# Optimization experiments

Measured on AMD Instinct MI355X. Metric: run time of the kernel, lower is better.

Reference implementation:

```python
import jax, jax.numpy as jnp
import numpy as np

B = 1024          # batch
L = 200           # max_len (history length)
DIM = 64          # args.dim
ITEM_NUM = 100000 # vocab; table has ITEM_NUM+1 rows, row 0 = padding
NEG = -1e15       # mask additive constant used by the original module


def setup_inputs() -> dict:
    key = jax.random.key(0)
    k1, k2, k3, k4, k5 = jax.random.split(key, 5)
    log_seqs = jax.random.randint(k1, (B, L), 0, ITEM_NUM + 1)          # item ids, 0 = pad
    pred = jax.random.randint(k2, (B, 1), 0, ITEM_NUM + 1)              # gather targets
    item_emb = jax.random.normal(k3, (ITEM_NUM + 1, DIM), jnp.float32) * 0.02
    item_emb = item_emb.at[0].set(0.0)                                  # padding_idx=0
    attn_key = jax.random.uniform(k4, (1, DIM), jnp.float32)            # self.key (torch.rand init)
    pos_emb = jax.random.normal(k5, (L, DIM), jnp.float32) * 0.02       # positional table
    return {"log_seqs": log_seqs, "pred": pred, "item_emb": item_emb,
            "attn_key": attn_key, "pos_emb": pos_emb}


def reference(log_seqs, pred, item_emb, attn_key, pos_emb):
    dim = item_emb.shape[1]
    mask = log_seqs != 0                                  # [B, L] True where valid
    # log2feats (model='P2MAMO', dropout p=0 -> identity)
    seqs = item_emb[log_seqs] * jnp.sqrt(jnp.float32(dim))  # [B, L, D]
    seqs = seqs + pos_emb[None, :, :]
    seqs = seqs * mask[..., None]                         # zero out padded positions
    # single-query dot-product attention pooling with learned key
    sim = jnp.einsum('bld,d->bl', seqs, attn_key[0])      # (q*k).sum(-1)
    sim = sim + jnp.where(mask, 0.0, NEG)                 # sim + (~mask)*-1e15
    attn = jax.nn.softmax(sim, axis=-1)                   # [B, L]
    Q = jnp.einsum('bld,bl->bd', seqs, attn)              # [B, D]
    # training path (isEval=False): full-vocab logits -> softmax -> gather
    logits = Q @ item_emb.T                               # [B, V+1]
    probs = jax.nn.softmax(logits, axis=-1)
    pos_logits = jnp.take_along_axis(probs, pred, axis=1) # [B, 1]
    return pos_logits
```

## Files before the change

kernel.cpp:

```cpp
#include <hip/hip_runtime.h>
#include <math.h>

#define B_TOT   1024
#define L_SEQ   200
#define DIM     64
#define VOCAB   100001
#define NEG_BIG (-1e15f)
#define SEQ_ST16 66
#define LOG2E   1.4426950408889634f
#define EB_SLACK_ROWS 512

typedef __bf16 bf16x8 __attribute__((ext_vector_type(8)));
typedef float  f32x4  __attribute__((ext_vector_type(4)));

static __device__ __forceinline__ float fast_exp2(float x) {
    return __builtin_amdgcn_exp2f(x);
}

__global__ __launch_bounds__(256) void pool_kernel(
    const int*   __restrict__ log_seqs,
    const float* __restrict__ item_emb,
    const float* __restrict__ attn_key,
    const float* __restrict__ pos_emb,
    float*       __restrict__ Q,
    __bf16*      __restrict__ Qb,
    __bf16*      __restrict__ Eb)
{
    const int b    = blockIdx.x;
    const int t    = threadIdx.x;
    const int wave = t >> 6;
    const int lane = t & 63;

    __shared__ unsigned short s_seq16[L_SEQ][SEQ_ST16];
    __shared__ float s_attn[L_SEQ];
    __shared__ float s_red[4];
    __shared__ float s_q[4][DIM];

    float sim = -INFINITY;
    if (t < L_SEQ) {
        const int id = log_seqs[(long)b * L_SEQ + t];
        if (id == 0) {
            sim = NEG_BIG;
            const ushort2 z = make_ushort2(0, 0);
            #pragma unroll
            for (int i = 0; i < DIM / 2; ++i)
                *(ushort2*)&s_seq16[t][2 * i] = z;
        } else {
            float acc = 0.f;
            const float4* e4 = (const float4*)(item_emb + (long)id * DIM);
            const float4* p4 = (const float4*)(pos_emb + t * DIM);
            #pragma unroll
            for (int i = 0; i < DIM / 4; ++i) {
                const float4 e = e4[i];
                const float4 p = p4[i];
                float4 f;
                f.x = fmaf(8.f, e.x, p.x);
                f.y = fmaf(8.f, e.y, p.y);
                f.z = fmaf(8.f, e.z, p.z);
                f.w = fmaf(8.f, e.w, p.w);
                const __bf16 h0 = (__bf16)f.x, h1 = (__bf16)f.y;
                const __bf16 h2 = (__bf16)f.z, h3 = (__bf16)f.w;
                ushort2 u0, u1;
                u0.x = __builtin_bit_cast(unsigned short, h0);
                u0.y = __builtin_bit_cast(unsigned short, h1);
                u1.x = __builtin_bit_cast(unsigned short, h2);
                u1.y = __builtin_bit_cast(unsigned short, h3);
                *(ushort2*)&s_seq16[t][4 * i]     = u0;
                *(ushort2*)&s_seq16[t][4 * i + 2] = u1;
                acc += f.x * attn_key[4*i+0] + f.y * attn_key[4*i+1]
                     + f.z * attn_key[4*i+2] + f.w * attn_key[4*i+3];
            }
            sim = acc;
        }
    }

    float m = sim;
    #pragma unroll
    for (int off = 32; off > 0; off >>= 1) m = fmaxf(m, __shfl_xor(m, off));
    if (lane == 0) s_red[wave] = m;
    __syncthreads();
    m = fmaxf(fmaxf(s_red[0], s_red[1]), fmaxf(s_red[2], s_red[3]));
    __syncthreads();

    float p = (t < L_SEQ) ? __expf(sim - m) : 0.f;
    if (t < L_SEQ) s_attn[t] = p;
    float ls = p;
    #pragma unroll
    for (int off = 32; off > 0; off >>= 1) ls += __shfl_xor(ls, off);
    if (lane == 0) s_red[wave] = ls;
    __syncthreads();
    const float inv = 1.0f / (s_red[0] + s_red[1] + s_red[2] + s_red[3]);

    float q = 0.f;
    const int l0 = wave * (L_SEQ / 4);
    #pragma unroll 2
    for (int l = l0; l < l0 + (L_SEQ / 4); ++l) {
        const unsigned int ui = (unsigned int)s_seq16[l][lane] << 16;
        q = fmaf(s_attn[l], __builtin_bit_cast(float, ui), q);
    }
    s_q[wave][lane] = q;
    __syncthreads();

    if (t < DIM) {
        const float qq = (s_q[0][t] + s_q[1][t] + s_q[2][t] + s_q[3][t]) * inv;
        Q[b * DIM + t]  = qq;
        Qb[b * DIM + t] = (__bf16)(qq * LOG2E);
    }

    {
        const long n8 = ((long)VOCAB * DIM) / 8;
        for (long g = (long)b * 256 + t; g < n8; g += (long)gridDim.x * 256) {
            const long i = g * 8;
            const float4 f0 = ((const float4*)(item_emb + i))[0];
            const float4 f1 = ((const float4*)(item_emb + i))[1];
            bf16x8 o;
            o[0] = (__bf16)f0.x; o[1] = (__bf16)f0.y; o[2] = (__bf16)f0.z; o[3] = (__bf16)f0.w;
            o[4] = (__bf16)f1.x; o[5] = (__bf16)f1.y; o[6] = (__bf16)f1.z; o[7] = (__bf16)f1.w;
            *(bf16x8*)(Eb + i) = o;
        }
    }
}

#define NC        128
#define NBG       8
#define VT_TOTAL  6251
#define VT_FULL   6250
#define VT_PER    49
#define VT_STEP   (16 * 16 * DIM)

__global__ __launch_bounds__(256) void logits_mfma(
    const __bf16* __restrict__ Eb,
    const __bf16* __restrict__ Qb,
    float*        __restrict__ partials)
{
    const int bid   = blockIdx.x;
    const int xcd   = bid & 7;
    const int idx   = bid >> 3;
    const int chunk = xcd + 8 * (idx >> 3);
    const int bg    = idx & 7;
    const int wave  = threadIdx.x >> 6;
    const int lane  = threadIdx.x & 63;
    const int r16   = lane & 15;
    const int hi    = lane >> 4;

    __shared__ float s_part[4][128];

    bf16x8 a[8][2];
    #pragma unroll
    for (int t = 0; t < 8; ++t)
        #pragma unroll
        for (int s = 0; s < 2; ++s)
            a[t][s] = *(const bf16x8*)(Qb + ((bg*128 + t*16 + r16) * DIM) + s*32 + hi*8);

    const int vt0    = chunk * VT_PER;
    const int vt_end = min(vt0 + VT_PER, VT_TOTAL);
    int vt = vt0 + wave;

    float ssum[8][4];
    #pragma unroll
    for (int t = 0; t < 8; ++t)
        #pragma unroll
        for (int r = 0; r < 4; ++r) ssum[t][r] = 0.f;

    #define DO_TILE(c0, c1, v) do {                                           \
        if ((v) < VT_FULL) {                                                  \
            _Pragma("unroll")                                                 \
            for (int t = 0; t < 8; ++t) {                                     \
                f32x4 acc = {0.f, 0.f, 0.f, 0.f};                             \
                acc = __builtin_amdgcn_mfma_f32_16x16x32_bf16(a[t][0], c0, acc, 0, 0, 0); \
                acc = __builtin_amdgcn_mfma_f32_16x16x32_bf16(a[t][1], c1, acc, 0, 0, 0); \
                _Pragma("unroll")                                             \
                for (int r = 0; r < 4; ++r) ssum[t][r] += fast_exp2(acc[r]);  \
            }                                                                 \
        } else {                                                              \
            const bool valid = ((v) * 16 + r16) < VOCAB;                      \
            _Pragma("unroll")                                                 \
            for (int t = 0; t < 8; ++t) {                                     \
                f32x4 acc = {0.f, 0.f, 0.f, 0.f};                             \
                acc = __builtin_amdgcn_mfma_f32_16x16x32_bf16(a[t][0], c0, acc, 0, 0, 0); \
                acc = __builtin_amdgcn_mfma_f32_16x16x32_bf16(a[t][1], c1, acc, 0, 0, 0); \
                _Pragma("unroll")                                             \
                for (int r = 0; r < 4; ++r) ssum[t][r] += valid ? fast_exp2(acc[r]) : 0.f; \
            }                                                                 \
        }                                                                     \
    } while (0)

    const __bf16* base = Eb + ((size_t)vt * 16 + r16) * DIM + hi * 8;
    const __bf16* pA = base;
    const __bf16* pB = base + 4  * 16 * DIM;
    const __bf16* pC = base + 8  * 16 * DIM;
    const __bf16* pD = base + 12 * 16 * DIM;

    bf16x8 A0 = *(const bf16x8*)pA, A1 = *(const bf16x8*)(pA + 32);
    bf16x8 B0 = *(const bf16x8*)pB, B1 = *(const bf16x8*)(pB + 32);
    bf16x8 C0 = *(const bf16x8*)pC, C1 = *(const bf16x8*)(pC + 32);
    bf16x8 D0 = *(const bf16x8*)pD, D1 = *(const bf16x8*)(pD + 32);

    for (;;) {
        DO_TILE(A0, A1, vt);
        if (vt + 4 < vt_end) DO_TILE(B0, B1, vt + 4);
        pA += VT_STEP; pB += VT_STEP;
        A0 = *(const bf16x8*)pA; A1 = *(const bf16x8*)(pA + 32);
        B0 = *(const bf16x8*)pB; B1 = *(const bf16x8*)(pB + 32);
        vt += 8;
        if (vt >= vt_end) break;

        DO_TILE(C0, C1, vt);
        if (vt + 4 < vt_end) DO_TILE(D0, D1, vt + 4);
        pC += VT_STEP; pD += VT_STEP;
        C0 = *(const bf16x8*)pC; C1 = *(const bf16x8*)(pC + 32);
        D0 = *(const bf16x8*)pD; D1 = *(const bf16x8*)(pD + 32);
        vt += 8;
        if (vt >= vt_end) break;
    }
    #undef DO_TILE

    #pragma unroll
    for (int t = 0; t < 8; ++t)
        #pragma unroll
        for (int r = 0; r < 4; ++r) {
            float v = ssum[t][r];
            v += __shfl_xor(v, 1);
            v += __shfl_xor(v, 2);
            v += __shfl_xor(v, 4);
            v += __shfl_xor(v, 8);
            ssum[t][r] = v;
        }

    if (r16 == 0) {
        #pragma unroll
        for (int t = 0; t < 8; ++t)
            #pragma unroll
            for (int r = 0; r < 4; ++r)
                s_part[wave][t * 16 + hi * 4 + r] = ssum[t][r];
    }
    __syncthreads();

    if (threadIdx.x < 128) {
        const int i = threadIdx.x;
        const float v = s_part[0][i] + s_part[1][i] + s_part[2][i] + s_part[3][i];
        partials[(size_t)chunk * B_TOT + bg * 128 + i] = v;
    }
}

__global__ __launch_bounds__(256) void finalize_kernel(
    const float* __restrict__ Q,
    const float* __restrict__ item_emb,
    const int*   __restrict__ pred,
    const float* __restrict__ partials,
    float*       __restrict__ out)
{
    const int b = blockIdx.x * 256 + threadIdx.x;

    float S = 0.f;
    for (int c = 0; c < NC; ++c)
        S += partials[(size_t)c * B_TOT + b];

    const int pv = pred[b];
    float acc = 0.f;
    const float4* e4 = (const float4*)(item_emb + (long)pv * DIM);
    const float4* q4 = (const float4*)(Q + b * DIM);
    #pragma unroll
    for (int i = 0; i < DIM / 4; ++i) {
        const float4 e = e4[i];
        const float4 q = q4[i];
        acc += e.x*q.x + e.y*q.y + e.z*q.z + e.w*q.w;
    }
    out[b] = __expf(acc) / S;
}

extern "C" void kernel_launch(void* const* d_in, const int* in_sizes, int n_in,
                              void* d_out, int out_size, void* d_ws, size_t ws_size,
                              hipStream_t stream)
{
    const int*   log_seqs = (const int*)  d_in[0];
    const int*   pred     = (const int*)  d_in[1];
    const float* item_emb = (const float*)d_in[2];
    const float* attn_key = (const float*)d_in[3];
    const float* pos_emb  = (const float*)d_in[4];
    float*       out      = (float*)d_out;

    char* ws = (char*)d_ws;
    const size_t eb_bytes = (size_t)(VOCAB + EB_SLACK_ROWS) * DIM * 2;
    __bf16* Eb       = (__bf16*)ws;
    __bf16* Qb       = (__bf16*)(ws + eb_bytes);
    float*  Qf       = (float*) (ws + eb_bytes + (size_t)B_TOT * DIM * 2);
    float*  partials = (float*) ((char*)Qf + (size_t)B_TOT * DIM * 4);

    pool_kernel<<<B_TOT, 256, 0, stream>>>(log_seqs, item_emb, attn_key, pos_emb, Qf, Qb, Eb);
    logits_mfma<<<NBG * NC, 256, 0, stream>>>(Eb, Qb, partials);
    finalize_kernel<<<B_TOT / 256, 256, 0, stream>>>(Qf, item_emb, pred, partials, out);
}
```

Before: 64.06 us.

## Fuse fp32-to-bf16 table conversion into the logits MFMA loop

```diff
diff --git a/kernel.cpp b/kernel.cpp
--- a/kernel.cpp
+++ b/kernel.cpp
@@ -8,13 +8,19 @@
 #define NEG_BIG (-1e15f)
 #define SEQ_ST16 66
 #define LOG2E   1.4426950408889634f
-#define EB_SLACK_ROWS 512
 
 typedef __bf16 bf16x8 __attribute__((ext_vector_type(8)));
 typedef float  f32x4  __attribute__((ext_vector_type(4)));
 
 static __device__ __forceinline__ float fast_exp2(float x) {
     return __builtin_amdgcn_exp2f(x);
+}
+
+static __device__ __forceinline__ bf16x8 cvt_bf16x8(const float4 a, const float4 b) {
+    bf16x8 o;
+    o[0] = (__bf16)a.x; o[1] = (__bf16)a.y; o[2] = (__bf16)a.z; o[3] = (__bf16)a.w;
+    o[4] = (__bf16)b.x; o[5] = (__bf16)b.y; o[6] = (__bf16)b.z; o[7] = (__bf16)b.w;
+    return o;
 }
 
 __global__ __launch_bounds__(256) void pool_kernel(
@@ -23,8 +29,7 @@
     const float* __restrict__ attn_key,
     const float* __restrict__ pos_emb,
     float*       __restrict__ Q,
-    __bf16*      __restrict__ Qb,
-    __bf16*      __restrict__ Eb)
+    __bf16*      __restrict__ Qb)
 {
     const int b    = blockIdx.x;
     const int t    = threadIdx.x;
@@ -106,19 +111,6 @@
         Q[b * DIM + t]  = qq;
         Qb[b * DIM + t] = (__bf16)(qq * LOG2E);
     }
-
-    {
-        const long n8 = ((long)VOCAB * DIM) / 8;
-        for (long g = (long)b * 256 + t; g < n8; g += (long)gridDim.x * 256) {
-            const long i = g * 8;
-            const float4 f0 = ((const float4*)(item_emb + i))[0];
-            const float4 f1 = ((const float4*)(item_emb + i))[1];
-            bf16x8 o;
-            o[0] = (__bf16)f0.x; o[1] = (__bf16)f0.y; o[2] = (__bf16)f0.z; o[3] = (__bf16)f0.w;
-            o[4] = (__bf16)f1.x; o[5] = (__bf16)f1.y; o[6] = (__bf16)f1.z; o[7] = (__bf16)f1.w;
-            *(bf16x8*)(Eb + i) = o;
-        }
-    }
 }
 
 #define NC        128
@@ -126,10 +118,9 @@
 #define VT_TOTAL  6251
 #define VT_FULL   6250
 #define VT_PER    49
-#define VT_STEP   (16 * 16 * DIM)
-
-__global__ __launch_bounds__(256) void logits_mfma(
-    const __bf16* __restrict__ Eb,
+
+__global__ __launch_bounds__(256, 3) void logits_mfma(
+    const float*  __restrict__ E,
     const __bf16* __restrict__ Qb,
     float*        __restrict__ partials)
 {
@@ -161,6 +152,15 @@
     for (int t = 0; t < 8; ++t)
         #pragma unroll
         for (int r = 0; r < 4; ++r) ssum[t][r] = 0.f;
+
+    #define LOADB(dst, vti) do {                                              \
+        const int _row = min((vti) * 16 + r16, VOCAB - 1);                    \
+        const float* _p = E + (size_t)_row * DIM + hi * 8;                    \
+        dst[0] = ((const float4*)_p)[0];                                      \
+        dst[1] = ((const float4*)_p)[1];                                      \
+        dst[2] = ((const float4*)(_p + 32))[0];                               \
+        dst[3] = ((const float4*)(_p + 32))[1];                               \
+    } while (0)
 
     #define DO_TILE(c0, c1, v) do {                                           \
         if ((v) < VT_FULL) {                                                  \
@@ -185,35 +185,32 @@
         }                                                                     \
     } while (0)
 
-    const __bf16* base = Eb + ((size_t)vt * 16 + r16) * DIM + hi * 8;
-    const __bf16* pA = base;
-    const __bf16* pB = base + 4  * 16 * DIM;
-    const __bf16* pC = base + 8  * 16 * DIM;
-    const __bf16* pD = base + 12 * 16 * DIM;
-
-    bf16x8 A0 = *(const bf16x8*)pA, A1 = *(const bf16x8*)(pA + 32);
-    bf16x8 B0 = *(const bf16x8*)pB, B1 = *(const bf16x8*)(pB + 32);
-    bf16x8 C0 = *(const bf16x8*)pC, C1 = *(const bf16x8*)(pC + 32);
-    bf16x8 D0 = *(const bf16x8*)pD, D1 = *(const bf16x8*)(pD + 32);
-
-    for (;;) {
-        DO_TILE(A0, A1, vt);
-        if (vt + 4 < vt_end) DO_TILE(B0, B1, vt + 4);
-        pA += VT_STEP; pB += VT_STEP;
-        A0 = *(const bf16x8*)pA; A1 = *(const bf16x8*)(pA + 32);
-        B0 = *(const bf16x8*)pB; B1 = *(const bf16x8*)(pB + 32);
+    float4 bA[4], bB[4];
+    LOADB(bA, vt);
+    LOADB(bB, vt + 4);
+
+    while (vt < vt_end) {
+        float4 cA[4], cB[4];
+        #pragma unroll
+        for (int i = 0; i < 4; ++i) { cA[i] = bA[i]; cB[i] = bB[i]; }
+        const int v0 = vt, v1 = vt + 4;
         vt += 8;
-        if (vt >= vt_end) break;
-
-        DO_TILE(C0, C1, vt);
-        if (vt + 4 < vt_end) DO_TILE(D0, D1, vt + 4);
-        pC += VT_STEP; pD += VT_STEP;
-        C0 = *(const bf16x8*)pC; C1 = *(const bf16x8*)(pC + 32);
-        D0 = *(const bf16x8*)pD; D1 = *(const bf16x8*)(pD + 32);
-        vt += 8;
-        if (vt >= vt_end) break;
+        LOADB(bA, vt);
+        LOADB(bB, vt + 4);
+
+        {
+            const bf16x8 c0 = cvt_bf16x8(cA[0], cA[1]);
+            const bf16x8 c1 = cvt_bf16x8(cA[2], cA[3]);
+            DO_TILE(c0, c1, v0);
+        }
+        if (v1 < vt_end) {
+            const bf16x8 c0 = cvt_bf16x8(cB[0], cB[1]);
+            const bf16x8 c1 = cvt_bf16x8(cB[2], cB[3]);
+            DO_TILE(c0, c1, v1);
+        }
     }
     #undef DO_TILE
+    #undef LOADB
 
     #pragma unroll
     for (int t = 0; t < 8; ++t)
@@ -281,13 +278,11 @@
     float*       out      = (float*)d_out;
 
     char* ws = (char*)d_ws;
-    const size_t eb_bytes = (size_t)(VOCAB + EB_SLACK_ROWS) * DIM * 2;
-    __bf16* Eb       = (__bf16*)ws;
-    __bf16* Qb       = (__bf16*)(ws + eb_bytes);
-    float*  Qf       = (float*) (ws + eb_bytes + (size_t)B_TOT * DIM * 2);
+    __bf16* Qb       = (__bf16*)ws;
+    float*  Qf       = (float*) (ws + (size_t)B_TOT * DIM * 2);
     float*  partials = (float*) ((char*)Qf + (size_t)B_TOT * DIM * 4);
 
-    pool_kernel<<<B_TOT, 256, 0, stream>>>(log_seqs, item_emb, attn_key, pos_emb, Qf, Qb, Eb);
-    logits_mfma<<<NBG * NC, 256, 0, stream>>>(Eb, Qb, partials);
+    pool_kernel<<<B_TOT, 256, 0, stream>>>(log_seqs, item_emb, attn_key, pos_emb, Qf, Qb);
+    logits_mfma<<<NBG * NC, 256, 0, stream>>>(item_emb, Qb, partials);
     finalize_kernel<<<B_TOT / 256, 256, 0, stream>>>(Qf, item_emb, pred, partials, out);
 }
```

Result: slower. 115.9 us (+80.9%).

## Stage item-embedding tiles through LDS with async global_load_lds ring buffer

Applied to the files above, without the earlier changes.

```diff
diff --git a/kernel.cpp b/kernel.cpp
--- a/kernel.cpp
+++ b/kernel.cpp
@@ -12,6 +12,9 @@
 
 typedef __bf16 bf16x8 __attribute__((ext_vector_type(8)));
 typedef float  f32x4  __attribute__((ext_vector_type(4)));
+
+#define GLB_AS __attribute__((address_space(1)))
+#define LDS_AS __attribute__((address_space(3)))
 
 static __device__ __forceinline__ float fast_exp2(float x) {
     return __builtin_amdgcn_exp2f(x);
@@ -126,7 +129,8 @@
 #define VT_TOTAL  6251
 #define VT_FULL   6250
 #define VT_PER    49
-#define VT_STEP   (16 * 16 * DIM)
+#define SLOTS     5
+#define SLOT_B    2048
 
 __global__ __launch_bounds__(256) void logits_mfma(
     const __bf16* __restrict__ Eb,
@@ -143,7 +147,10 @@
     const int r16   = lane & 15;
     const int hi    = lane >> 4;
 
+    __shared__ char  s_stage[4 * SLOTS * SLOT_B];
     __shared__ float s_part[4][128];
+
+    char* wbase = s_stage + wave * (SLOTS * SLOT_B);
 
     bf16x8 a[8][2];
     #pragma unroll
@@ -161,6 +168,18 @@
     for (int t = 0; t < 8; ++t)
         #pragma unroll
         for (int r = 0; r < 4; ++r) ssum[t][r] = 0.f;
+
+    const __bf16* src = Eb + ((size_t)vt * 16 + r16) * DIM + hi * 8;
+
+    #define STAGE(slot, sp) do {                                              \
+        char* _d = wbase + (slot) * SLOT_B;                                   \
+        __builtin_amdgcn_global_load_lds(                                     \
+            (const GLB_AS void*)(const void*)(sp),                            \
+            (LDS_AS void*)(void*)_d, 16, 0, 0);                               \
+        __builtin_amdgcn_global_load_lds(                                     \
+            (const GLB_AS void*)(const void*)((sp) + 32),                     \
+            (LDS_AS void*)(void*)(_d + 1024), 16, 0, 0);                      \
+    } while (0)
 
     #define DO_TILE(c0, c1, v) do {                                           \
         if ((v) < VT_FULL) {                                                  \
@@ -185,35 +204,26 @@
         }                                                                     \
     } while (0)
 
-    const __bf16* base = Eb + ((size_t)vt * 16 + r16) * DIM + hi * 8;
-    const __bf16* pA = base;
-    const __bf16* pB = base + 4  * 16 * DIM;
-    const __bf16* pC = base + 8  * 16 * DIM;
-    const __bf16* pD = base + 12 * 16 * DIM;
-
-    bf16x8 A0 = *(const bf16x8*)pA, A1 = *(const bf16x8*)(pA + 32);
-    bf16x8 B0 = *(const bf16x8*)pB, B1 = *(const bf16x8*)(pB + 32);
-    bf16x8 C0 = *(const bf16x8*)pC, C1 = *(const bf16x8*)(pC + 32);
-    bf16x8 D0 = *(const bf16x8*)pD, D1 = *(const bf16x8*)(pD + 32);
-
-    for (;;) {
-        DO_TILE(A0, A1, vt);
-        if (vt + 4 < vt_end) DO_TILE(B0, B1, vt + 4);
-        pA += VT_STEP; pB += VT_STEP;
-        A0 = *(const bf16x8*)pA; A1 = *(const bf16x8*)(pA + 32);
-        B0 = *(const bf16x8*)pB; B1 = *(const bf16x8*)(pB + 32);
-        vt += 8;
-        if (vt >= vt_end) break;
-
-        DO_TILE(C0, C1, vt);
-        if (vt + 4 < vt_end) DO_TILE(D0, D1, vt + 4);
-        pC += VT_STEP; pD += VT_STEP;
-        C0 = *(const bf16x8*)pC; C1 = *(const bf16x8*)(pC + 32);
-        D0 = *(const bf16x8*)pD; D1 = *(const bf16x8*)(pD + 32);
-        vt += 8;
-        if (vt >= vt_end) break;
+    STAGE(0, src);
+    STAGE(1, src + 4096);
+    STAGE(2, src + 8192);
+    STAGE(3, src + 12288);
+
+    int slot_r = 0, slot_w = 4;
+    while (vt < vt_end) {
+        STAGE(slot_w, src + 16384);
+        if (++slot_w == SLOTS) slot_w = 0;
+        src += 4096;
+        asm volatile("s_waitcnt vmcnt(8)" ::: "memory");
+        const char* rb = wbase + slot_r * SLOT_B + (size_t)lane * 16;
+        const bf16x8 c0 = *(const bf16x8*)rb;
+        const bf16x8 c1 = *(const bf16x8*)(rb + 1024);
+        if (++slot_r == SLOTS) slot_r = 0;
+        DO_TILE(c0, c1, vt);
+        vt += 4;
     }
     #undef DO_TILE
+    #undef STAGE
 
     #pragma unroll
     for (int t = 0; t < 8; ++t)
```

New measurement: 70.29 us. 9.7% more time.

## Split logits blocks into single-wave blocks and drop shared-memory reduction

Applied to the files above, without the earlier changes.

```diff
diff --git a/kernel.cpp b/kernel.cpp
--- a/kernel.cpp
+++ b/kernel.cpp
@@ -126,25 +126,22 @@
 #define VT_TOTAL  6251
 #define VT_FULL   6250
 #define VT_PER    49
-#define VT_STEP   (16 * 16 * DIM)
-
-__global__ __launch_bounds__(256) void logits_mfma(
+
+__global__ __launch_bounds__(64) void logits_mfma(
     const __bf16* __restrict__ Eb,
     const __bf16* __restrict__ Qb,
     float*        __restrict__ partials)
 {
     const int bid   = blockIdx.x;
     const int xcd   = bid & 7;
-    const int idx   = bid >> 3;
-    const int chunk = xcd + 8 * (idx >> 3);
-    const int bg    = idx & 7;
-    const int wave  = threadIdx.x >> 6;
-    const int lane  = threadIdx.x & 63;
+    const int sub   = bid >> 3;
+    const int wslot = sub & 3;
+    const int bg    = (sub >> 2) & 7;
+    const int chunk = xcd + 8 * (sub >> 5);
+    const int lane  = threadIdx.x;
     const int r16   = lane & 15;
     const int hi    = lane >> 4;
 
-    __shared__ float s_part[4][128];
-
     bf16x8 a[8][2];
     #pragma unroll
     for (int t = 0; t < 8; ++t)
@@ -154,7 +151,7 @@
 
     const int vt0    = chunk * VT_PER;
     const int vt_end = min(vt0 + VT_PER, VT_TOTAL);
-    int vt = vt0 + wave;
+    int vt = vt0 + wslot;
 
     float ssum[8][4];
     #pragma unroll
@@ -185,33 +182,26 @@
         }                                                                     \
     } while (0)
 
-    const __bf16* base = Eb + ((size_t)vt * 16 + r16) * DIM + hi * 8;
-    const __bf16* pA = base;
-    const __bf16* pB = base + 4  * 16 * DIM;
-    const __bf16* pC = base + 8  * 16 * DIM;
-    const __bf16* pD = base + 12 * 16 * DIM;
-
-    bf16x8 A0 = *(const bf16x8*)pA, A1 = *(const bf16x8*)(pA + 32);
-    bf16x8 B0 = *(const bf16x8*)pB, B1 = *(const bf16x8*)(pB + 32);
-    bf16x8 C0 = *(const bf16x8*)pC, C1 = *(const bf16x8*)(pC + 32);
-    bf16x8 D0 = *(const bf16x8*)pD, D1 = *(const bf16x8*)(pD + 32);
-
-    for (;;) {
-        DO_TILE(A0, A1, vt);
-        if (vt + 4 < vt_end) DO_TILE(B0, B1, vt + 4);
-        pA += VT_STEP; pB += VT_STEP;
-        A0 = *(const bf16x8*)pA; A1 = *(const bf16x8*)(pA + 32);
-        B0 = *(const bf16x8*)pB; B1 = *(const bf16x8*)(pB + 32);
+    const __bf16* p = Eb + ((size_t)vt * 16 + r16) * DIM + hi * 8;
+
+    bf16x8 b0, b1, d0, d1;
+    b0 = *(const bf16x8*)p;
+    b1 = *(const bf16x8*)(p + 32);
+    d0 = *(const bf16x8*)(p + 4096);
+    d1 = *(const bf16x8*)(p + 4096 + 32);
+
+    while (vt < vt_end) {
+        const bf16x8 c00 = b0, c01 = b1, c10 = d0, c11 = d1;
+        const int v0 = vt, v1 = vt + 4;
         vt += 8;
-        if (vt >= vt_end) break;
-
-        DO_TILE(C0, C1, vt);
-        if (vt + 4 < vt_end) DO_TILE(D0, D1, vt + 4);
-        pC += VT_STEP; pD += VT_STEP;
-        C0 = *(const bf16x8*)pC; C1 = *(const bf16x8*)(pC + 32);
-        D0 = *(const bf16x8*)pD; D1 = *(const bf16x8*)(pD + 32);
-        vt += 8;
-        if (vt >= vt_end) break;
+        p += 8192;
+        b0 = *(const bf16x8*)p;
+        b1 = *(const bf16x8*)(p + 32);
+        d0 = *(const bf16x8*)(p + 4096);
+        d1 = *(const bf16x8*)(p + 4096 + 32);
+
+        DO_TILE(c00, c01, v0);
+        if (v1 < vt_end) DO_TILE(c10, c11, v1);
     }
     #undef DO_TILE
 
@@ -228,18 +218,14 @@
         }
 
     if (r16 == 0) {
+        const int slot = chunk * 4 + wslot;
         #pragma unroll
         for (int t = 0; t < 8; ++t)
             #pragma unroll
-            for (int r = 0; r < 4; ++r)
-                s_part[wave][t * 16 + hi * 4 + r] = ssum[t][r];
-    }
-    __syncthreads();
-
-    if (threadIdx.x < 128) {
-        const int i = threadIdx.x;
-        const float v = s_part[0][i] + s_part[1][i] + s_part[2][i] + s_part[3][i];
-        partials[(size_t)chunk * B_TOT + bg * 128 + i] = v;
+            for (int r = 0; r < 4; ++r) {
+                const int row = bg * 128 + t * 16 + hi * 4 + r;
+                partials[(size_t)slot * B_TOT + row] = ssum[t][r];
+            }
     }
 }
 
@@ -253,8 +239,8 @@
     const int b = blockIdx.x * 256 + threadIdx.x;
 
     float S = 0.f;
-    for (int c = 0; c < NC; ++c)
-        S += partials[(size_t)c * B_TOT + b];
+    for (int w = 0; w < NC * 4; ++w)
+        S += partials[(size_t)w * B_TOT + b];
 
     const int pv = pred[b];
     float acc = 0.f;
@@ -288,6 +274,6 @@
     float*  partials = (float*) ((char*)Qf + (size_t)B_TOT * DIM * 4);
 
     pool_kernel<<<B_TOT, 256, 0, stream>>>(log_seqs, item_emb, attn_key, pos_emb, Qf, Qb, Eb);
-    logits_mfma<<<NBG * NC, 256, 0, stream>>>(Eb, Qb, partials);
+    logits_mfma<<<NBG * NC * 4, 64, 0, stream>>>(Eb, Qb, partials);
     finalize_kernel<<<B_TOT / 256, 256, 0, stream>>>(Qf, item_emb, pred, partials, out);
 }
```

Measured after the change: 80.57 us. 25.8% more time.
